# Kernel optimization log

Hardware: AMD Instinct MI355X
Metric: run time of the kernel (lower is better)

The kernel has to match this reference:

```python
import jax, jax.numpy as jnp
import numpy as np

N_QUBITS = 9
C64 = jnp.complex64

PZ = jnp.array([[1, 0], [0, -1]], dtype=C64)
PX = jnp.array([[0, 1], [1, 0]], dtype=C64)
PY = jnp.array([[0, -1j], [1j, 0]], dtype=C64)
CNOT = jnp.array([[1, 0, 0, 0], [0, 1, 0, 0], [0, 0, 0, 1], [0, 0, 1, 0]], dtype=C64).reshape(2, 2, 2, 2)


def _rx(t):
    c = jnp.cos(t / 2).astype(C64)
    s = jnp.sin(t / 2).astype(C64)
    return jnp.stack([jnp.stack([c, -1j * s]), jnp.stack([-1j * s, c])])


def _ry(t):
    c = jnp.cos(t / 2).astype(C64)
    s = jnp.sin(t / 2).astype(C64)
    return jnp.stack([jnp.stack([c, -s]), jnp.stack([s, c])])


def _ap1(state, g, q):
    # apply 2x2 gate g on qubit axis q of state with shape (2,)*n
    return jnp.moveaxis(jnp.tensordot(g, state, axes=((1,), (q,))), 0, q)


def _ap2(state, g, q1, q2):
    return jnp.moveaxis(jnp.tensordot(g, state, axes=((2, 3), (q1, q2))), (0, 1), (q1, q2))


def _simulate(x, w, n, Denc, D):
    state = jnp.zeros((2,) * n, dtype=C64).at[(0,) * n].set(1.0)
    idx = 0
    for j in range(n):
        state = _ap1(state, _rx(x[idx]), j)
        state = _ap1(state, _ry(x[idx + 1]), j)
        idx += 2
    for _ in range(Denc):
        for j in range(n):
            state = _ap2(state, CNOT, j, (j + 1) % n)
        for j in range(n):
            state = _ap1(state, _ry(x[idx]), j)
            idx += 1
    idx = 0
    for j in range(n):
        state = _ap1(state, _rx(w[idx]), j)
        state = _ap1(state, _ry(w[idx + 1]), j)
        idx += 2
    for _ in range(D):
        for j in range(n):
            state = _ap2(state, CNOT, j, (j + 1) % n)
        for j in range(n):
            state = _ap1(state, _ry(w[idx]), j)
            idx += 1
    return state


def _expZ0(state):
    return jnp.real(jnp.vdot(state, _ap1(state, PZ, 0)))


def _expvals(state, n, ngroups):
    # E[p, q] = <Pauli_p on qubit q>; observable i -> qubit i%n, pauli (i//n)%3 (Z,X,Y)
    E = jnp.stack([jnp.stack([jnp.real(jnp.vdot(state, _ap1(state, P, q))) for q in range(n)])
                   for P in (PZ, PX, PY)])
    return jnp.concatenate([E[g % 3] for g in range(ngroups)])


def _forward(inp, wq, wk, wv):
    B, S, d = inp.shape
    n = N_QUBITS
    Denc = d // n - 2
    D = wq.shape[0] // n - 2
    flat = jnp.swapaxes(inp, 0, 1).reshape(S * B, d)  # matches torch transpose(0,1).reshape
    qk_fn = jax.vmap(lambda x, w: _expZ0(_simulate(x, w, n, Denc, D)), in_axes=(0, None))
    v_fn = jax.vmap(lambda x: _expvals(_simulate(x, wv, n, Denc, D), n, Denc + 2))
    Q = qk_fn(flat, wq).reshape(S, B, 1).swapaxes(0, 1).astype(inp.dtype)  # (B,S,1)
    K = qk_fn(flat, wk).reshape(S, B, 1).swapaxes(0, 1).astype(inp.dtype)
    V = v_fn(flat).reshape(S, B, d).swapaxes(0, 1).astype(inp.dtype)       # (B,S,d)
    alpha = jnp.exp(-(Q[:, :, None, :] - K[:, None, :, :]) ** 2)  # (B,S,S,1)
    alpha = alpha / jnp.sum(alpha, axis=2, keepdims=True)
    return inp + jnp.sum(alpha * V[:, None, :, :], axis=2)


def setup_inputs() -> dict:
    key = jax.random.key(0)
    k1, k2, k3, k4 = jax.random.split(key, 4)
    B, S, n, Denc, D = 48, 96, 9, 4, 8
    d = n * (Denc + 2)          # 54
    wdim = n * (D + 2)          # 90
    pi4 = np.float32(np.pi / 4)
    return {
        "input": jax.random.normal(k1, (B, S, d), dtype=jnp.float32),
        "params_Q": pi4 * (2 * jax.random.normal(k2, (wdim,), dtype=jnp.float32) - 1),
        "params_K": pi4 * (2 * jax.random.normal(k3, (wdim,), dtype=jnp.float32) - 1),
        "params_V": pi4 * (2 * jax.random.normal(k4, (wdim,), dtype=jnp.float32) - 1),
    }


def reference(input, params_Q, params_K, params_V):
    return _forward(input, params_Q, params_K, params_V)
```

## Files before the change

### kernel.cpp

```cpp
#include <hip/hip_runtime.h>
#include <math.h>

#define B_DIM  48
#define S_DIM  96
#define D_DIM  54
#define DENC   4
#define DVAR   8
#define NFLAT  (B_DIM * S_DIM)

typedef _Float16 h2 __attribute__((ext_vector_type(2)));

__device__ __forceinline__ int h2i(h2 v) { return __builtin_bit_cast(int, v); }
__device__ __forceinline__ h2  i2h(int v) { return __builtin_bit_cast(h2, v); }

__device__ __forceinline__ int pk_mul(int a, int b) {
    int d;
    asm("v_pk_mul_f16 %0, %1, %2" : "=v"(d) : "v"(a), "v"(b));
    return d;
}
__device__ __forceinline__ int pk_fma(int a, int b, int c) {
    int d;
    asm("v_pk_fma_f16 %0, %1, %2, %3" : "=v"(d) : "v"(a), "v"(b), "v"(c));
    return d;
}

template<int LM>
__device__ __forceinline__ int lxi(int x, int lane) {
    if constexpr (LM == 1)       return __builtin_amdgcn_update_dpp(x, x, 0xB1, 0xF, 0xF, true);
    else if constexpr (LM == 2)  return __builtin_amdgcn_update_dpp(x, x, 0x4E, 0xF, 0xF, true);
    else if constexpr (LM == 4)  return __builtin_amdgcn_ds_swizzle(x, 0x101F);
    else if constexpr (LM == 8)  return __builtin_amdgcn_update_dpp(x, x, 0x128, 0xF, 0xF, true);
    else if constexpr (LM == 16) return __builtin_amdgcn_ds_swizzle(x, 0x401F);
    else {
        auto r = __builtin_amdgcn_permlane32_swap(x, x, false, false);
        return (lane & 32) ? r[0] : r[1];
    }
}
template<int LM>
__device__ __forceinline__ float lx(float v, int lane) {
    return __int_as_float(lxi<LM>(__float_as_int(v), lane));
}

__device__ __forceinline__ float wave_sum(float v, int lane) {
    v += lx<32>(v, lane);
    v += lx<16>(v, lane);
    v += lx<8>(v, lane);
    v += lx<4>(v, lane);
    v += lx<2>(v, lane);
    v += lx<1>(v, lane);
    return v;
}


__device__ __forceinline__ int hswapi(int p) {
    return __builtin_amdgcn_alignbit(p, p, 16);
}

__device__ __forceinline__ void ring(h2 st[8], int lane) {
    const int gray = (lane ^ (lane >> 1)) << 2;
#pragma unroll
    for (int r = 0; r < 8; ++r)
        st[r] = i2h(__builtin_amdgcn_ds_bpermute(gray, h2i(st[r])));
    {
        const bool c0 = (lane & 1) != 0;
#pragma unroll
        for (int r = 0; r < 4; ++r) {
            h2 a = st[r], b = st[r + 4];
            st[r]     = c0 ? b : a;
            st[r + 4] = c0 ? a : b;
        }
    }
    { h2 t = st[4]; st[4] = st[6]; st[6] = t; }
    { h2 t = st[5]; st[5] = st[7]; st[7] = t; }
    { h2 t = st[2]; st[2] = st[3]; st[3] = t; }
    { h2 t = st[6]; st[6] = st[7]; st[7] = t; }
#pragma unroll
    for (int r = 1; r < 8; r += 2)
        st[r] = i2h(lxi<32>(h2i(st[r]), lane));
}

template<int BJ>
__device__ __forceinline__ void rot_ry(h2 st[8], int c2i, int s2i, int lane) {
    if constexpr (BJ >= 3) {
        constexpr int lm = 1 << (BJ - 3);
        const int sg = (lane & lm) ? s2i : (s2i ^ 0x80008000);
#pragma unroll
        for (int r = 0; r < 8; ++r) {
            int p = lxi<lm>(h2i(st[r]), lane);
            st[r] = i2h(pk_fma(p, sg, pk_mul(h2i(st[r]), c2i)));
        }
    } else {
        constexpr int M = 1 << BJ;
        const int ns2 = s2i ^ 0x80008000;
#pragma unroll
        for (int r = 0; r < 8; ++r) {
            if ((r & M) == 0) {
                int a = h2i(st[r]), b = h2i(st[r + M]);
                st[r]     = i2h(pk_fma(b, ns2, pk_mul(a, c2i)));
                st[r + M] = i2h(pk_fma(a, s2i, pk_mul(b, c2i)));
            }
        }
    }
}

template<int BJ>
__device__ __forceinline__ void rot_rx(h2 st[8], int c2i, int s2i, int lane) {
    const int sm = s2i ^ 0x80000000;
    if constexpr (BJ >= 3) {
        constexpr int lm = 1 << (BJ - 3);
#pragma unroll
        for (int r = 0; r < 8; ++r) {
            int p = lxi<lm>(h2i(st[r]), lane);
            st[r] = i2h(pk_fma(hswapi(p), sm, pk_mul(h2i(st[r]), c2i)));
        }
    } else {
        constexpr int M = 1 << BJ;
#pragma unroll
        for (int r = 0; r < 8; ++r) {
            if ((r & M) == 0) {
                int a = h2i(st[r]), b = h2i(st[r + M]);
                st[r]     = i2h(pk_fma(hswapi(b), sm, pk_mul(a, c2i)));
                st[r + M] = i2h(pk_fma(hswapi(a), sm, pk_mul(b, c2i)));
            }
        }
    }
}

#define INITQ(j) { rot_rx<8 - (j)>(st, cc[2 * (j)],     ss[2 * (j)],     lane);  \
                   rot_ry<8 - (j)>(st, cc[2 * (j) + 1], ss[2 * (j) + 1], lane); }

__device__ __forceinline__ void ry_layer(h2 st[8], const int* pc, const int* ps, int lane) {
    rot_ry<8>(st, pc[0], ps[0], lane);
    rot_ry<7>(st, pc[1], ps[1], lane);
    rot_ry<6>(st, pc[2], ps[2], lane);
    rot_ry<5>(st, pc[3], ps[3], lane);
    rot_ry<4>(st, pc[4], ps[4], lane);
    rot_ry<3>(st, pc[5], ps[5], lane);
    rot_ry<2>(st, pc[6], ps[6], lane);
    rot_ry<1>(st, pc[7], ps[7], lane);
    rot_ry<0>(st, pc[8], ps[8], lane);
}

template<int BJ>
__device__ __forceinline__ void expv(const h2 st[8], int lane, float& ez, float& ex, float& ey) {
    ez = ex = ey = 0.f;
    if constexpr (BJ >= 3) {
        constexpr int lm = 1 << (BJ - 3);
        const float sgn = (lane & lm) ? -1.f : 1.f;
#pragma unroll
        for (int r = 0; r < 8; ++r) {
            h2 p = i2h(lxi<lm>(h2i(st[r]), lane));
            float x = (float)st[r].x, y = (float)st[r].y;
            float px = (float)p.x,   py = (float)p.y;
            ez += sgn * (x * x + y * y);
            ex += x * px + y * py;
            ey += sgn * (x * py - y * px);
        }
    } else {
        constexpr int M = 1 << BJ;
#pragma unroll
        for (int r = 0; r < 8; ++r) {
            if ((r & M) == 0) {
                float ax = (float)st[r].x,     ay = (float)st[r].y;
                float bx = (float)st[r + M].x, by = (float)st[r + M].y;
                ez += (ax * ax + ay * ay) - (bx * bx + by * by);
                ex += 2.f * (ax * bx + ay * by);
                ey += 2.f * (ax * by - ay * bx);
            }
        }
    }
    ez = wave_sum(ez, lane); ex = wave_sum(ex, lane); ey = wave_sum(ey, lane);
}

__global__ __launch_bounds__(64) void enc_kernel(
    const float* __restrict__ inp, int* __restrict__ encOut)
{
    __shared__ int csc[54];
    __shared__ int css[54];

    const int lane = threadIdx.x;
    const int fi   = blockIdx.x;
    const int b = fi % B_DIM, s = fi / B_DIM;
    const float* x = inp + ((size_t)b * S_DIM + s) * D_DIM;

    if (lane < 54) {
        float ang = x[lane];
        float sn, cn; sincosf(0.5f * ang, &sn, &cn);
        _Float16 hc = (_Float16)cn, hs = (_Float16)sn;
        h2 c2 = {hc, hc}, s2 = {hs, hs};
        csc[lane] = h2i(c2);
        css[lane] = h2i(s2);
    }

    h2 st[8];
#pragma unroll
    for (int r = 0; r < 8; ++r) st[r] = i2h(0);
    if (lane == 0) { h2 one = {(_Float16)1.f, (_Float16)0.f}; st[0] = one; }

    {
        const int* cc = csc; const int* ss = css;
        INITQ(0) INITQ(1) INITQ(2) INITQ(3) INITQ(4)
        INITQ(5) INITQ(6) INITQ(7) INITQ(8)
        const int* pc = csc + 18;
        const int* ps = css + 18;
#pragma unroll 1
        for (int L = 0; L < DENC; ++L) {
            ring(st, lane);
            ry_layer(st, pc, ps, lane);
            pc += 9; ps += 9;
        }
    }

    int* dst = encOut + (size_t)fi * 512;
#pragma unroll
    for (int r = 0; r < 8; ++r)
        dst[r * 64 + lane] = h2i(st[r]);
}

__global__ __launch_bounds__(64) void var_kernel(
    const int* __restrict__ encIn,
    const float* __restrict__ wq, const float* __restrict__ wk, const float* __restrict__ wv,
    float* __restrict__ outQ, float* __restrict__ outK, float* __restrict__ outV)
{
    __shared__ int csc[90];
    __shared__ int css[90];

    const int lane = threadIdx.x;
    const int gbl  = blockIdx.x;
    const int cid  = gbl % 3;
    const int fi   = gbl / 3;
    const float* w = (cid == 0) ? wq : (cid == 1) ? wk : wv;

    for (int k = lane; k < 90; k += 64) {
        float ang = w[k];
        float sn, cn; sincosf(0.5f * ang, &sn, &cn);
        _Float16 hc = (_Float16)cn, hs = (_Float16)sn;
        h2 c2 = {hc, hc}, s2 = {hs, hs};
        csc[k] = h2i(c2);
        css[k] = h2i(s2);
    }

    h2 st[8];
    const int* src = encIn + (size_t)fi * 512;
#pragma unroll
    for (int r = 0; r < 8; ++r)
        st[r] = i2h(src[r * 64 + lane]);

    {
        const int* cc = csc; const int* ss = css;
        INITQ(0) INITQ(1) INITQ(2) INITQ(3) INITQ(4)
        INITQ(5) INITQ(6) INITQ(7) INITQ(8)
        const int* pc = csc + 18;
        const int* ps = css + 18;
#pragma unroll 1
        for (int L = 0; L < DVAR - 1; ++L) {
            ring(st, lane);
            ry_layer(st, pc, ps, lane);
            pc += 9; ps += 9;
        }
        ring(st, lane);
        if (cid < 2) {
            rot_ry<8>(st, pc[0], ps[0], lane);
        } else {
            ry_layer(st, pc, ps, lane);
        }
    }

    if (cid < 2) {
        float p = 0.f;
#pragma unroll
        for (int r = 0; r < 8; ++r) {
            float xx = (float)st[r].x, yy = (float)st[r].y;
            p += xx * xx + yy * yy;
        }
        p = (lane & 32) ? -p : p;
        p = wave_sum(p, lane);
        if (lane == 0) { if (cid == 0) outQ[fi] = p; else outK[fi] = p; }
    } else {
        float* vrow = outV + (size_t)fi * D_DIM;
#define EXPQ(q) { float ez, ex, ey; expv<8 - (q)>(st, lane, ez, ex, ey);            \
                  if (lane == 0) { vrow[(q)] = ez; vrow[9 + (q)] = ex;              \
                                   vrow[18 + (q)] = ey; vrow[27 + (q)] = ez;        \
                                   vrow[36 + (q)] = ex; vrow[45 + (q)] = ey; } }
        EXPQ(0) EXPQ(1) EXPQ(2) EXPQ(3) EXPQ(4)
        EXPQ(5) EXPQ(6) EXPQ(7) EXPQ(8)
#undef EXPQ
    }
}

__global__ __launch_bounds__(256) void attn_kernel(
    const float* __restrict__ inp, const float* __restrict__ Q,
    const float* __restrict__ K,   const float* __restrict__ V,
    float* __restrict__ out)
{
    __shared__ float w4[4][S_DIM];
    const int warp = threadIdx.x >> 6;
    const int t    = threadIdx.x & 63;
    const int bi   = blockIdx.x * 4 + warp;
    const int b    = bi / S_DIM;
    const int i    = bi % S_DIM;
    float* w = w4[warp];

    const float q = Q[i * B_DIM + b];
    float e0, e1 = 0.f;
    {
        float d0 = q - K[t * B_DIM + b];
        e0 = expf(-d0 * d0);
        w[t] = e0;
        if (t < S_DIM - 64) {
            float d1 = q - K[(t + 64) * B_DIM + b];
            e1 = expf(-d1 * d1);
            w[t + 64] = e1;
        }
    }
    float ps = wave_sum(e0 + e1, t);
    const float inv = 1.f / ps;

    if (t < D_DIM) {
        float acc = 0.f;
        for (int j = 0; j < S_DIM; ++j)
            acc += w[j] * V[(size_t)(j * B_DIM + b) * D_DIM + t];
        size_t o = (size_t)bi * D_DIM + t;
        out[o] = inp[o] + acc * inv;
    }
}

extern "C" void kernel_launch(void* const* d_in, const int* in_sizes, int n_in,
                              void* d_out, int out_size, void* d_ws, size_t ws_size,
                              hipStream_t stream)
{
    (void)in_sizes; (void)n_in; (void)out_size; (void)ws_size;
    const float* inp = (const float*)d_in[0];
    const float* wq  = (const float*)d_in[1];
    const float* wk  = (const float*)d_in[2];
    const float* wv  = (const float*)d_in[3];
    float* outp = (float*)d_out;

    float* Qw  = (float*)d_ws;
    float* Kw  = Qw + NFLAT;
    float* Vw  = Kw + NFLAT;
    int*   Enc = (int*)(Vw + (size_t)NFLAT * D_DIM);

    enc_kernel<<<NFLAT, 64, 0, stream>>>(inp, Enc);
    var_kernel<<<NFLAT * 3, 64, 0, stream>>>(Enc, wq, wk, wv, Qw, Kw, Vw);
    attn_kernel<<<NFLAT / 4, 256, 0, stream>>>(inp, Qw, Kw, Vw, outp);
}
```

Baseline: 108.8 us.

## Fold lane-32 exchange into bpermute addresses and precompute weight sincos once

```diff
diff --git a/kernel.cpp b/kernel.cpp
--- a/kernel.cpp
+++ b/kernel.cpp
@@ -56,11 +56,32 @@
     return __builtin_amdgcn_alignbit(p, p, 16);
 }
 
-__device__ __forceinline__ void ring(h2 st[8], int lane) {
-    const int gray = (lane ^ (lane >> 1)) << 2;
-#pragma unroll
-    for (int r = 0; r < 8; ++r)
-        st[r] = i2h(__builtin_amdgcn_ds_bpermute(gray, h2i(st[r])));
+__device__ __forceinline__ h2 bp(int addr, h2 v) {
+    return i2h(__builtin_amdgcn_ds_bpermute(addr, h2i(v)));
+}
+
+struct RingAddr { int aA, aB, aC, aD; };
+__device__ __forceinline__ RingAddr make_ring_addr(int lane) {
+    const int gray   = (lane ^ (lane >> 1)) << 2;
+    const int gray48 = gray ^ 192;
+    const bool c0 = (lane & 1) != 0;
+    RingAddr ra;
+    ra.aA = gray;
+    ra.aB = gray48;
+    ra.aC = c0 ? gray : gray48;
+    ra.aD = c0 ? gray48 : gray;
+    return ra;
+}
+
+__device__ __forceinline__ void ring(h2 st[8], const RingAddr& ra, int lane) {
+    st[0] = bp(ra.aD, st[0]);
+    st[1] = bp(ra.aB, st[1]);
+    st[2] = bp(ra.aC, st[2]);
+    st[3] = bp(ra.aA, st[3]);
+    st[4] = bp(ra.aC, st[4]);
+    st[5] = bp(ra.aB, st[5]);
+    st[6] = bp(ra.aD, st[6]);
+    st[7] = bp(ra.aA, st[7]);
     {
         const bool c0 = (lane & 1) != 0;
 #pragma unroll
@@ -74,9 +95,6 @@
     { h2 t = st[5]; st[5] = st[7]; st[7] = t; }
     { h2 t = st[2]; st[2] = st[3]; st[3] = t; }
     { h2 t = st[6]; st[6] = st[7]; st[7] = t; }
-#pragma unroll
-    for (int r = 1; r < 8; r += 2)
-        st[r] = i2h(lxi<32>(h2i(st[r]), lane));
 }
 
 template<int BJ>
@@ -172,6 +190,21 @@
     ez = wave_sum(ez, lane); ex = wave_sum(ex, lane); ey = wave_sum(ey, lane);
 }
 
+__global__ __launch_bounds__(256) void prep_kernel(
+    const float* __restrict__ wq, const float* __restrict__ wk, const float* __restrict__ wv,
+    int* __restrict__ wcc, int* __restrict__ wss)
+{
+    int k = blockIdx.x * 256 + threadIdx.x;
+    if (k >= 270) return;
+    const float* p = (k < 90) ? wq : (k < 180) ? wk : wv;
+    float ang = p[k % 90];
+    float sn, cn; sincosf(0.5f * ang, &sn, &cn);
+    _Float16 hc = (_Float16)cn, hs = (_Float16)sn;
+    h2 c2 = {hc, hc}, s2 = {hs, hs};
+    wcc[k] = h2i(c2);
+    wss[k] = h2i(s2);
+}
+
 __global__ __launch_bounds__(64) void enc_kernel(
     const float* __restrict__ inp, int* __restrict__ encOut)
 {
@@ -191,6 +224,8 @@
         csc[lane] = h2i(c2);
         css[lane] = h2i(s2);
     }
+
+    const RingAddr ra = make_ring_addr(lane);
 
     h2 st[8];
 #pragma unroll
@@ -205,7 +240,7 @@
         const int* ps = css + 18;
 #pragma unroll 1
         for (int L = 0; L < DENC; ++L) {
-            ring(st, lane);
+            ring(st, ra, lane);
             ry_layer(st, pc, ps, lane);
             pc += 9; ps += 9;
         }
@@ -219,7 +254,7 @@
 
 __global__ __launch_bounds__(64) void var_kernel(
     const int* __restrict__ encIn,
-    const float* __restrict__ wq, const float* __restrict__ wk, const float* __restrict__ wv,
+    const int* __restrict__ wcc, const int* __restrict__ wss,
     float* __restrict__ outQ, float* __restrict__ outK, float* __restrict__ outV)
 {
     __shared__ int csc[90];
@@ -229,16 +264,13 @@
     const int gbl  = blockIdx.x;
     const int cid  = gbl % 3;
     const int fi   = gbl / 3;
-    const float* w = (cid == 0) ? wq : (cid == 1) ? wk : wv;
 
     for (int k = lane; k < 90; k += 64) {
-        float ang = w[k];
-        float sn, cn; sincosf(0.5f * ang, &sn, &cn);
-        _Float16 hc = (_Float16)cn, hs = (_Float16)sn;
-        h2 c2 = {hc, hc}, s2 = {hs, hs};
-        csc[k] = h2i(c2);
-        css[k] = h2i(s2);
-    }
+        csc[k] = wcc[cid * 90 + k];
+        css[k] = wss[cid * 90 + k];
+    }
+
+    const RingAddr ra = make_ring_addr(lane);
 
     h2 st[8];
     const int* src = encIn + (size_t)fi * 512;
@@ -254,11 +286,11 @@
         const int* ps = css + 18;
 #pragma unroll 1
         for (int L = 0; L < DVAR - 1; ++L) {
-            ring(st, lane);
+            ring(st, ra, lane);
             ry_layer(st, pc, ps, lane);
             pc += 9; ps += 9;
         }
-        ring(st, lane);
+        ring(st, ra, lane);
         if (cid < 2) {
             rot_ry<8>(st, pc[0], ps[0], lane);
         } else {
@@ -340,8 +372,11 @@
     float* Kw  = Qw + NFLAT;
     float* Vw  = Kw + NFLAT;
     int*   Enc = (int*)(Vw + (size_t)NFLAT * D_DIM);
-
+    int*   Wcc = Enc + (size_t)NFLAT * 512;
+    int*   Wss = Wcc + 270;
+
+    prep_kernel<<<2, 256, 0, stream>>>(wq, wk, wv, Wcc, Wss);
     enc_kernel<<<NFLAT, 64, 0, stream>>>(inp, Enc);
-    var_kernel<<<NFLAT * 3, 64, 0, stream>>>(Enc, wq, wk, wv, Qw, Kw, Vw);
+    var_kernel<<<NFLAT * 3, 64, 0, stream>>>(Enc, Wcc, Wss, Qw, Kw, Vw);
     attn_kernel<<<NFLAT / 4, 256, 0, stream>>>(inp, Qw, Kw, Vw, outp);
 }
```

Result: no change. 109.7 us (+0.9%).
